# Optimization experiments

Hardware: AMD Instinct MI355X
Metric: run time of the kernel (lower is better)

Reference implementation:

```python
import jax, jax.numpy as jnp
import numpy as np

INPUT_SIZE = 768
HIDDEN = 384


def _gru_dir(x, W_ih, W_hh, b_ih, b_hh, reverse):
    """Single-direction GRU, torch gate order (r, z, n).
    x: [B, S, D] -> outputs [B, S, H]."""
    B = x.shape[0]
    H = W_hh.shape[1]
    # Precompute input projections for all timesteps: [B, S, 3H] -> [S, B, 3H]
    xw = jnp.swapaxes(x @ W_ih.T + b_ih, 0, 1)

    def step(h, xw_t):
        gh = h @ W_hh.T + b_hh
        xr, xz, xn = jnp.split(xw_t, 3, axis=-1)
        hr, hz, hn = jnp.split(gh, 3, axis=-1)
        r = jax.nn.sigmoid(xr + hr)
        z = jax.nn.sigmoid(xz + hz)
        n = jnp.tanh(xn + r * hn)
        h_new = (1.0 - z) * n + z * h
        return h_new, h_new

    h0 = jnp.zeros((B, H), dtype=x.dtype)
    _, hs = jax.lax.scan(step, h0, xw, reverse=reverse)  # [S, B, H]
    return jnp.swapaxes(hs, 0, 1)


def setup_inputs() -> dict:
    key = jax.random.key(0)
    ks = jax.random.split(key, 12)
    B, S, D, H = 32, 512, INPUT_SIZE, HIDDEN
    s_ih = 1.0 / np.sqrt(H)
    u = lambda k, shape: jax.random.uniform(k, shape, jnp.float32, -s_ih, s_ih)
    inp = {
        "ip": jax.random.normal(ks[0], (B, S, D), jnp.float32),
        # forward-direction GRU params
        "W_ih_f": u(ks[1], (3 * H, D)),
        "W_hh_f": u(ks[2], (3 * H, H)),
        "b_ih_f": u(ks[3], (3 * H,)),
        "b_hh_f": u(ks[4], (3 * H,)),
        # backward-direction GRU params
        "W_ih_b": u(ks[5], (3 * H, D)),
        "W_hh_b": u(ks[6], (3 * H, H)),
        "b_ih_b": u(ks[7], (3 * H,)),
        "b_hh_b": u(ks[8], (3 * H,)),
        # sentence attention params (input_dim = 2H)
        "W_attn": u(ks[9], (2 * H, 2 * H)),
        "b_attn": u(ks[10], (2 * H,)),
        "context": jax.random.normal(ks[11], (2 * H,), jnp.float32) * 0.05,
    }
    return inp


def reference(ip, W_ih_f, W_hh_f, b_ih_f, b_hh_f,
              W_ih_b, W_hh_b, b_ih_b, b_hh_b,
              W_attn, b_attn, context):
    # BiGRU encode: concat forward & backward hidden states -> [B, S, 2H]
    h_f = _gru_dir(ip, W_ih_f, W_hh_f, b_ih_f, b_hh_f, reverse=False)
    h_b = _gru_dir(ip, W_ih_b, W_hh_b, b_ih_b, b_hh_b, reverse=True)
    out = jnp.concatenate([h_f, h_b], axis=-1)
    # Additive attention pooling over sentences
    scores = jnp.tanh(out @ W_attn.T + b_attn) @ context  # [B, S]
    attn = jax.nn.softmax(scores, axis=1)
    doc_embeds = jnp.einsum("bs,bsd->bd", attn, out)  # [B, 2H]
    return doc_embeds
```

## Files before the change

kernel.cpp:

```cpp
#include <hip/hip_runtime.h>
#include <hip/hip_fp16.h>

typedef _Float16 half2_t __attribute__((ext_vector_type(2)));
typedef _Float16 half4_t __attribute__((ext_vector_type(4)));
typedef _Float16 half8_t __attribute__((ext_vector_type(8)));
typedef float floatx4 __attribute__((ext_vector_type(4)));

#define B_   32
#define S_   512
#define D_   768
#define H_   384
#define H3_  1152
#define M_   (B_*S_)
#define N2_  (2*H3_)
#define TWOH_ 768
#define NWG_DIR 6
#define JSPAN 64

__device__ __forceinline__ int4 load16_cc(const void* p) {
  int4 r;
  unsigned long long a = (unsigned long long)p;
  asm volatile("global_load_dwordx4 %0, %1, off sc0 sc1\n\t"
               "s_waitcnt vmcnt(0)"
               : "=v"(r) : "v"(a) : "memory");
  return r;
}
__device__ __forceinline__ void load16_cc3(const void* p0, const void* p1, const void* p2,
                                           int4& v0, int4& v1, int4& v2) {
  unsigned long long a0 = (unsigned long long)p0;
  unsigned long long a1 = (unsigned long long)p1;
  unsigned long long a2 = (unsigned long long)p2;
  asm volatile("global_load_dwordx4 %0, %3, off sc0 sc1\n\t"
               "global_load_dwordx4 %1, %4, off sc0 sc1\n\t"
               "global_load_dwordx4 %2, %5, off sc0 sc1\n\t"
               "s_waitcnt vmcnt(0)"
               : "=&v"(v0), "=&v"(v1), "=&v"(v2)
               : "v"(a0), "v"(a1), "v"(a2) : "memory");
}
__device__ __forceinline__ void store8_cc(void* p, int2 v) {
  unsigned long long a = (unsigned long long)p;
  asm volatile("global_store_dwordx2 %0, %1, off sc0 sc1"
               :: "v"(a), "v"(v) : "memory");
}
__device__ __forceinline__ void wait_vm0() {
  asm volatile("s_waitcnt vmcnt(0)" ::: "memory");
}

__global__ void cvt_f32_f16_kernel(const float* __restrict__ src,
                                   _Float16* __restrict__ dst, int n4) {
  int i = blockIdx.x * blockDim.x + threadIdx.x;
  if (i >= n4) return;
  float4 v = ((const float4*)src)[i];
  half4_t h = {(_Float16)v.x, (_Float16)v.y, (_Float16)v.z, (_Float16)v.w};
  ((half4_t*)dst)[i] = h;
}

__global__ __launch_bounds__(256) void gemm_xw_kernel(
    const _Float16* __restrict__ A, const _Float16* __restrict__ Bm,
    const float* __restrict__ bias_f, const float* __restrict__ bias_b,
    _Float16* __restrict__ xw) {
  __shared__ _Float16 As[64][40];
  __shared__ _Float16 Bs[64][40];
  const int m0 = blockIdx.x * 64, n0 = blockIdx.y * 64;
  const int tid = threadIdx.x, lane = tid & 63, w = tid >> 6;
  const int wm = w >> 1, wn = w & 1;
  const int q = lane >> 4, c = lane & 15;
  floatx4 acc[2][2] = {};

  const int t = tid & 127;
  const int srow = t >> 1, skh = (t & 1) * 16;
  const _Float16* gsrc =
      (tid < 128 ? A + (size_t)(m0 + srow) * D_ : Bm + (size_t)(n0 + srow) * D_) + skh;
  _Float16* ldst = (tid < 128) ? &As[srow][skh] : &Bs[srow][skh];

  for (int k0 = 0; k0 < D_; k0 += 32) {
    half8_t v0 = *(const half8_t*)(gsrc + k0);
    half8_t v1 = *(const half8_t*)(gsrc + k0 + 8);
    __syncthreads();
    *(half8_t*)ldst = v0;
    *(half8_t*)(ldst + 8) = v1;
    __syncthreads();
    half8_t a0 = *(const half8_t*)&As[wm * 32 + c][q * 8];
    half8_t a1 = *(const half8_t*)&As[wm * 32 + 16 + c][q * 8];
    half8_t b0 = *(const half8_t*)&Bs[wn * 32 + c][q * 8];
    half8_t b1 = *(const half8_t*)&Bs[wn * 32 + 16 + c][q * 8];
    acc[0][0] = __builtin_amdgcn_mfma_f32_16x16x32_f16(a0, b0, acc[0][0], 0, 0, 0);
    acc[0][1] = __builtin_amdgcn_mfma_f32_16x16x32_f16(a0, b1, acc[0][1], 0, 0, 0);
    acc[1][0] = __builtin_amdgcn_mfma_f32_16x16x32_f16(a1, b0, acc[1][0], 0, 0, 0);
    acc[1][1] = __builtin_amdgcn_mfma_f32_16x16x32_f16(a1, b1, acc[1][1], 0, 0, 0);
  }
  for (int mi = 0; mi < 2; ++mi)
    for (int ni = 0; ni < 2; ++ni)
      for (int r = 0; r < 4; ++r) {
        int m = m0 + wm * 32 + mi * 16 + q * 4 + r;
        int n = n0 + wn * 32 + ni * 16 + c;
        int dir = n >= H3_;
        int nn = n - dir * H3_;
        float bv = dir ? bias_b[nn] : bias_f[nn];
        float vv = acc[mi][ni][r] + bv;
        int s = m & (S_ - 1), bb = m >> 9;
        xw[(((size_t)dir * S_ + s) * B_ + bb) * H3_ + nn] = (_Float16)vv;
      }
}

__global__ __launch_bounds__(512, 2) void gru_mfma_kernel(
    const _Float16* __restrict__ xw,
    const _Float16* __restrict__ Whh,
    const float* __restrict__ bhh_f, const float* __restrict__ bhh_b,
    _Float16* __restrict__ hglob,
    _Float16* __restrict__ out16,
    int* __restrict__ bar) {
  const int wg = blockIdx.x;
  const int dir = wg / NWG_DIR;
  const int wgj = wg % NWG_DIR;
  const int j0w = wgj * JSPAN;
  const int tid = threadIdx.x, lane = tid & 63, w = tid >> 6;
  const int bt = w & 1, jt = w >> 1;
  const int c = lane & 15, q = lane >> 4;

  __shared__ __align__(16) _Float16 hS[32 * 392];
  __shared__ __align__(16) float ghS[3 * 32 * 68];

  half8_t bfr[3][12];
  {
    const int jglob = j0w + jt * 16 + c;
#pragma unroll
    for (int g = 0; g < 3; ++g) {
      const _Float16* wp = Whh + ((size_t)dir * H3_ + g * H_ + jglob) * H_ + q * 8;
#pragma unroll
      for (int kt = 0; kt < 12; ++kt) bfr[g][kt] = *(const half8_t*)(wp + kt * 32);
    }
  }
  const float* bhh = dir ? bhh_b : bhh_f;
  const int gb = tid >> 4, jq = tid & 15;
  const int jg4 = j0w + jq * 4;
  float br[4], bz[4], bn[4], hc[4];
#pragma unroll
  for (int i = 0; i < 4; ++i) {
    br[i] = bhh[jg4 + i];
    bz[i] = bhh[H_ + jg4 + i];
    bn[i] = bhh[2 * H_ + jg4 + i];
    hc[i] = 0.f;
  }
  int* flg = bar + dir * 256;

  for (int step = 0; step < S_; ++step) {
    const int t = dir ? (S_ - 1 - step) : step;
    const int par = step & 1;

    const _Float16* xp = xw + (((size_t)dir * S_ + t) * B_ + gb) * H3_ + jg4;
    half4_t xr4 = *(const half4_t*)(xp);
    half4_t xz4 = *(const half4_t*)(xp + H_);
    half4_t xn4 = *(const half4_t*)(xp + 2 * H_);

    if (step > 0 && w == 0) {
      int v;
      do {
        v = (lane < NWG_DIR)
                ? __hip_atomic_load(&flg[lane * 16], __ATOMIC_RELAXED,
                                    __HIP_MEMORY_SCOPE_AGENT)
                : 0x7fffffff;
      } while (!__all(v >= step));
    }
    __syncthreads();

    {
      const _Float16* hb = hglob + ((size_t)dir * 2 + par) * B_ * H_;
      int g0 = tid, g1 = tid + 512, g2 = tid + 1024;
      int4 v0, v1, v2;
      load16_cc3(hb + (g0 / 48) * H_ + (g0 % 48) * 8,
                 hb + (g1 / 48) * H_ + (g1 % 48) * 8,
                 hb + (g2 / 48) * H_ + (g2 % 48) * 8, v0, v1, v2);
      *(int4*)&hS[(g0 / 48) * 392 + (g0 % 48) * 8] = v0;
      *(int4*)&hS[(g1 / 48) * 392 + (g1 % 48) * 8] = v1;
      *(int4*)&hS[(g2 / 48) * 392 + (g2 % 48) * 8] = v2;
    }
    __syncthreads();

    floatx4 a0 = {}, a1 = {}, a2 = {};
    {
      const _Float16* hrow = &hS[(bt * 16 + c) * 392 + q * 8];
#pragma unroll
      for (int kt = 0; kt < 12; ++kt) {
        half8_t af = *(const half8_t*)(hrow + kt * 32);
        a0 = __builtin_amdgcn_mfma_f32_16x16x32_f16(af, bfr[0][kt], a0, 0, 0, 0);
        a1 = __builtin_amdgcn_mfma_f32_16x16x32_f16(af, bfr[1][kt], a1, 0, 0, 0);
        a2 = __builtin_amdgcn_mfma_f32_16x16x32_f16(af, bfr[2][kt], a2, 0, 0, 0);
      }
    }
#pragma unroll
    for (int r = 0; r < 4; ++r) {
      int brow = bt * 16 + q * 4 + r;
      ghS[(0 * 32 + brow) * 68 + jt * 16 + c] = a0[r];
      ghS[(1 * 32 + brow) * 68 + jt * 16 + c] = a1[r];
      ghS[(2 * 32 + brow) * 68 + jt * 16 + c] = a2[r];
    }
    __syncthreads();

    floatx4 arv = *(floatx4*)&ghS[(0 * 32 + gb) * 68 + jq * 4];
    floatx4 azv = *(floatx4*)&ghS[(1 * 32 + gb) * 68 + jq * 4];
    floatx4 anv = *(floatx4*)&ghS[(2 * 32 + gb) * 68 + jq * 4];
    half4_t hh;
#pragma unroll
    for (int i = 0; i < 4; ++i) {
      float rr = 1.f / (1.f + __expf(-((float)xr4[i] + arv[i] + br[i])));
      float zz = 1.f / (1.f + __expf(-((float)xz4[i] + azv[i] + bz[i])));
      float u = (float)xn4[i] + rr * (anv[i] + bn[i]);
      float e = __expf(-2.f * u);
      float nv = (1.f - e) / (1.f + e);
      hc[i] = (1.f - zz) * nv + zz * hc[i];
      hh[i] = (_Float16)hc[i];
    }
    store8_cc(hglob + (((size_t)dir * 2 + (par ^ 1)) * B_ + gb) * H_ + jg4,
              __builtin_bit_cast(int2, hh));
    wait_vm0();
    __syncthreads();
    if (tid == 0)
      __hip_atomic_store(&flg[wgj * 16], step + 1, __ATOMIC_RELAXED,
                         __HIP_MEMORY_SCOPE_AGENT);
    *(half4_t*)&out16[((size_t)gb * S_ + t) * TWOH_ + dir * H_ + jg4] = hh;
  }
}

__global__ __launch_bounds__(256) void attn_score_kernel(
    const _Float16* __restrict__ A ,
    const _Float16* __restrict__ Bm ,
    const float* __restrict__ b_attn, const float* __restrict__ ctx,
    float* __restrict__ scores) {
  __shared__ _Float16 As[64][40];
  __shared__ _Float16 Bs[64][40];
  const int m0 = blockIdx.x * 64, n0 = blockIdx.y * 64;
  const int tid = threadIdx.x, lane = tid & 63, w = tid >> 6;
  const int wm = w >> 1, wn = w & 1;
  const int q = lane >> 4, c = lane & 15;
  floatx4 acc[2][2] = {};

  const int t = tid & 127;
  const int srow = t >> 1, skh = (t & 1) * 16;
  const _Float16* gsrc =
      (tid < 128 ? A + (size_t)(m0 + srow) * D_ : Bm + (size_t)(n0 + srow) * D_) + skh;
  _Float16* ldst = (tid < 128) ? &As[srow][skh] : &Bs[srow][skh];

  for (int k0 = 0; k0 < D_; k0 += 32) {
    half8_t v0 = *(const half8_t*)(gsrc + k0);
    half8_t v1 = *(const half8_t*)(gsrc + k0 + 8);
    __syncthreads();
    *(half8_t*)ldst = v0;
    *(half8_t*)(ldst + 8) = v1;
    __syncthreads();
    half8_t a0 = *(const half8_t*)&As[wm * 32 + c][q * 8];
    half8_t a1 = *(const half8_t*)&As[wm * 32 + 16 + c][q * 8];
    half8_t b0 = *(const half8_t*)&Bs[wn * 32 + c][q * 8];
    half8_t b1 = *(const half8_t*)&Bs[wn * 32 + 16 + c][q * 8];
    acc[0][0] = __builtin_amdgcn_mfma_f32_16x16x32_f16(a0, b0, acc[0][0], 0, 0, 0);
    acc[0][1] = __builtin_amdgcn_mfma_f32_16x16x32_f16(a0, b1, acc[0][1], 0, 0, 0);
    acc[1][0] = __builtin_amdgcn_mfma_f32_16x16x32_f16(a1, b0, acc[1][0], 0, 0, 0);
    acc[1][1] = __builtin_amdgcn_mfma_f32_16x16x32_f16(a1, b1, acc[1][1], 0, 0, 0);
  }
  for (int mi = 0; mi < 2; ++mi)
    for (int ni = 0; ni < 2; ++ni)
      for (int r = 0; r < 4; ++r) {
        int n = n0 + wn * 32 + ni * 16 + c;
        float vv = tanhf(acc[mi][ni][r] + b_attn[n]) * ctx[n];
        vv += __shfl_xor(vv, 1);
        vv += __shfl_xor(vv, 2);
        vv += __shfl_xor(vv, 4);
        vv += __shfl_xor(vv, 8);
        if (c == 0) {
          int m = m0 + wm * 32 + mi * 16 + q * 4 + r;
          atomicAdd(&scores[m], vv);
        }
      }
}

__global__ __launch_bounds__(256) void softmax_kernel(const float* __restrict__ scores,
                                                      float* __restrict__ attn) {
  const int b = blockIdx.x, tid = threadIdx.x;
  __shared__ float red[8];
  float s0 = scores[b * S_ + tid], s1 = scores[b * S_ + 256 + tid];
  float m = fmaxf(s0, s1);
  for (int off = 1; off < 64; off <<= 1) m = fmaxf(m, __shfl_xor(m, off));
  int wv = tid >> 6;
  if ((tid & 63) == 0) red[wv] = m;
  __syncthreads();
  m = fmaxf(fmaxf(red[0], red[1]), fmaxf(red[2], red[3]));
  float e0 = expf(s0 - m), e1 = expf(s1 - m);
  float sum = e0 + e1;
  for (int off = 1; off < 64; off <<= 1) sum += __shfl_xor(sum, off);
  if ((tid & 63) == 0) red[4 + wv] = sum;
  __syncthreads();
  sum = red[4] + red[5] + red[6] + red[7];
  float inv = 1.0f / sum;
  attn[b * S_ + tid] = e0 * inv;
  attn[b * S_ + 256 + tid] = e1 * inv;
}

__global__ __launch_bounds__(384) void doc_kernel(const float* __restrict__ attn,
                                                  const _Float16* __restrict__ out16,
                                                  float* __restrict__ dout) {
  const int b = blockIdx.x, tid = threadIdx.x;
  __shared__ float at[S_];
  for (int i = tid; i < S_; i += 384) at[i] = attn[b * S_ + i];
  __syncthreads();
  const half2_t* p = (const half2_t*)(out16 + (size_t)b * S_ * TWOH_) + tid;
  float acc0 = 0.f, acc1 = 0.f;
  for (int s = 0; s < S_; ++s) {
    half2_t h = p[(size_t)s * (TWOH_ / 2)];
    float wgt = at[s];
    acc0 += wgt * (float)h.x;
    acc1 += wgt * (float)h.y;
  }
  dout[b * TWOH_ + tid * 2] = acc0;
  dout[b * TWOH_ + tid * 2 + 1] = acc1;
}

extern "C" void kernel_launch(void* const* d_in, const int* in_sizes, int n_in,
                              void* d_out, int out_size, void* d_ws, size_t ws_size,
                              hipStream_t stream) {
  const float* ip     = (const float*)d_in[0];
  const float* W_ih_f = (const float*)d_in[1];
  const float* W_hh_f = (const float*)d_in[2];
  const float* b_ih_f = (const float*)d_in[3];
  const float* b_hh_f_p = (const float*)d_in[4];
  const float* W_ih_b = (const float*)d_in[5];
  const float* W_hh_b = (const float*)d_in[6];
  const float* b_ih_b = (const float*)d_in[7];
  const float* b_hh_b_p = (const float*)d_in[8];
  const float* W_attn = (const float*)d_in[9];
  const float* b_attn = (const float*)d_in[10];
  const float* context = (const float*)d_in[11];
  float* doc = (float*)d_out;

  char* ws = (char*)d_ws;
  size_t off = 0;
  auto alloc = [&](size_t bytes) {
    char* p = ws + off;
    off += (bytes + 255) & ~(size_t)255;
    return p;
  };
  _Float16* ip16    = (_Float16*)alloc((size_t)M_ * D_ * 2);
  _Float16* Wih16   = (_Float16*)alloc((size_t)N2_ * D_ * 2);
  _Float16* Whh16   = (_Float16*)alloc((size_t)2 * H3_ * H_ * 2);
  _Float16* Wattn16 = (_Float16*)alloc((size_t)TWOH_ * TWOH_ * 2);
  _Float16* xw      = (_Float16*)alloc((size_t)2 * S_ * B_ * H3_ * 2);
  _Float16* out16   = (_Float16*)alloc((size_t)B_ * S_ * TWOH_ * 2);
  _Float16* hglob   = (_Float16*)alloc((size_t)2 * 2 * B_ * H_ * 2);
  int*      bar     = (int*)alloc(4096);
  float* scores     = (float*)alloc((size_t)M_ * 4);
  float* attn       = (float*)alloc((size_t)M_ * 4);

  cvt_f32_f16_kernel<<<(M_ * D_ / 4 + 255) / 256, 256, 0, stream>>>(ip, ip16, M_ * D_ / 4);
  cvt_f32_f16_kernel<<<(H3_ * D_ / 4 + 255) / 256, 256, 0, stream>>>(W_ih_f, Wih16, H3_ * D_ / 4);
  cvt_f32_f16_kernel<<<(H3_ * D_ / 4 + 255) / 256, 256, 0, stream>>>(W_ih_b, Wih16 + (size_t)H3_ * D_, H3_ * D_ / 4);
  cvt_f32_f16_kernel<<<(H3_ * H_ / 4 + 255) / 256, 256, 0, stream>>>(W_hh_f, Whh16, H3_ * H_ / 4);
  cvt_f32_f16_kernel<<<(H3_ * H_ / 4 + 255) / 256, 256, 0, stream>>>(W_hh_b, Whh16 + (size_t)H3_ * H_, H3_ * H_ / 4);
  cvt_f32_f16_kernel<<<(TWOH_ * TWOH_ / 4 + 255) / 256, 256, 0, stream>>>(W_attn, Wattn16, TWOH_ * TWOH_ / 4);

  gemm_xw_kernel<<<dim3(M_ / 64, N2_ / 64), 256, 0, stream>>>(ip16, Wih16, b_ih_f, b_ih_b, xw);

  hipMemsetAsync(hglob, 0, (size_t)2 * 2 * B_ * H_ * 2, stream);
  hipMemsetAsync(bar, 0, 4096, stream);
  {
    const _Float16* xw_a = xw;
    const _Float16* whh_a = Whh16;
    const float* bf_a = b_hh_f_p;
    const float* bb_a = b_hh_b_p;
    _Float16* hg_a = hglob;
    _Float16* o16_a = out16;
    int* bar_a = bar;
    void* args[] = {(void*)&xw_a, (void*)&whh_a, (void*)&bf_a, (void*)&bb_a,
                    (void*)&hg_a, (void*)&o16_a, (void*)&bar_a};
    hipLaunchCooperativeKernel((const void*)gru_mfma_kernel, dim3(2 * NWG_DIR),
                               dim3(512), args, 0, stream);
  }

  hipMemsetAsync(scores, 0, (size_t)M_ * 4, stream);
  attn_score_kernel<<<dim3(M_ / 64, TWOH_ / 64), 256, 0, stream>>>(out16, Wattn16, b_attn, context, scores);

  softmax_kernel<<<B_, 256, 0, stream>>>(scores, attn);
  doc_kernel<<<B_, 384, 0, stream>>>(attn, out16, doc);
}
```

Before: 2.216 ms.

## Embed step tags in hidden-state words to replace flag barrier in GRU

The GRU recurrence now stores each pair of fp16 hidden values together with a step counter in one 64-bit word. Readers poll these words directly, so the separate per-workgroup flag array, the wait after the store, the extra block sync and the atomic flag store all go away. This is meant to cut the per-step inter-workgroup synchronisation latency. In addition, the K dimension of the hidden-state matmul is split across wave pairs, which halves the weight registers per thread and adds a two-way shared-memory reduction. The trade-offs are twice the bytes per hidden-state exchange and no zeroing of the exchange buffer, so correctness relies on stale tags never matching.

```diff
diff --git a/kernel.cpp b/kernel.cpp
--- a/kernel.cpp
+++ b/kernel.cpp
@@ -5,6 +5,7 @@
 typedef _Float16 half4_t __attribute__((ext_vector_type(4)));
 typedef _Float16 half8_t __attribute__((ext_vector_type(8)));
 typedef float floatx4 __attribute__((ext_vector_type(4)));
+typedef unsigned long long u64;
 
 #define B_   32
 #define S_   512
@@ -16,34 +17,38 @@
 #define TWOH_ 768
 #define NWG_DIR 6
 #define JSPAN 64
-
-__device__ __forceinline__ int4 load16_cc(const void* p) {
-  int4 r;
-  unsigned long long a = (unsigned long long)p;
-  asm volatile("global_load_dwordx4 %0, %1, off sc0 sc1\n\t"
-               "s_waitcnt vmcnt(0)"
-               : "=v"(r) : "v"(a) : "memory");
-  return r;
-}
-__device__ __forceinline__ void load16_cc3(const void* p0, const void* p1, const void* p2,
-                                           int4& v0, int4& v1, int4& v2) {
-  unsigned long long a0 = (unsigned long long)p0;
-  unsigned long long a1 = (unsigned long long)p1;
-  unsigned long long a2 = (unsigned long long)p2;
-  asm volatile("global_load_dwordx4 %0, %3, off sc0 sc1\n\t"
-               "global_load_dwordx4 %1, %4, off sc0 sc1\n\t"
-               "global_load_dwordx4 %2, %5, off sc0 sc1\n\t"
-               "s_waitcnt vmcnt(0)"
-               : "=&v"(v0), "=&v"(v1), "=&v"(v2)
-               : "v"(a0), "v"(a1), "v"(a2) : "memory");
-}
-__device__ __forceinline__ void store8_cc(void* p, int2 v) {
-  unsigned long long a = (unsigned long long)p;
+#define NCHUNK 6144
+
+__device__ __forceinline__ void store8_cc(void* p, u64 v) {
   asm volatile("global_store_dwordx2 %0, %1, off sc0 sc1"
-               :: "v"(a), "v"(v) : "memory");
-}
-__device__ __forceinline__ void wait_vm0() {
-  asm volatile("s_waitcnt vmcnt(0)" ::: "memory");
+               :: "v"((u64)p), "v"(v) : "memory");
+}
+__device__ __forceinline__ void load12_cc(const u64* base, int tid, u64 v[12]) {
+  u64 a0 = (u64)(base + tid);
+  u64 a1 = a0 + 1 * 4096, a2 = a0 + 2 * 4096, a3 = a0 + 3 * 4096;
+  u64 a4 = a0 + 4 * 4096, a5 = a0 + 5 * 4096, a6 = a0 + 6 * 4096;
+  u64 a7 = a0 + 7 * 4096, a8 = a0 + 8 * 4096, a9 = a0 + 9 * 4096;
+  u64 a10 = a0 + 10 * 4096, a11 = a0 + 11 * 4096;
+  asm volatile(
+      "global_load_dwordx2 %0, %12, off sc0 sc1\n\t"
+      "global_load_dwordx2 %1, %13, off sc0 sc1\n\t"
+      "global_load_dwordx2 %2, %14, off sc0 sc1\n\t"
+      "global_load_dwordx2 %3, %15, off sc0 sc1\n\t"
+      "global_load_dwordx2 %4, %16, off sc0 sc1\n\t"
+      "global_load_dwordx2 %5, %17, off sc0 sc1\n\t"
+      "global_load_dwordx2 %6, %18, off sc0 sc1\n\t"
+      "global_load_dwordx2 %7, %19, off sc0 sc1\n\t"
+      "global_load_dwordx2 %8, %20, off sc0 sc1\n\t"
+      "global_load_dwordx2 %9, %21, off sc0 sc1\n\t"
+      "global_load_dwordx2 %10, %22, off sc0 sc1\n\t"
+      "global_load_dwordx2 %11, %23, off sc0 sc1\n\t"
+      "s_waitcnt vmcnt(0)"
+      : "=&v"(v[0]), "=&v"(v[1]), "=&v"(v[2]), "=&v"(v[3]),
+        "=&v"(v[4]), "=&v"(v[5]), "=&v"(v[6]), "=&v"(v[7]),
+        "=&v"(v[8]), "=&v"(v[9]), "=&v"(v[10]), "=&v"(v[11])
+      : "v"(a0), "v"(a1), "v"(a2), "v"(a3), "v"(a4), "v"(a5),
+        "v"(a6), "v"(a7), "v"(a8), "v"(a9), "v"(a10), "v"(a11)
+      : "memory");
 }
 
 __global__ void cvt_f32_f16_kernel(const float* __restrict__ src,
@@ -107,28 +112,29 @@
     const _Float16* __restrict__ xw,
     const _Float16* __restrict__ Whh,
     const float* __restrict__ bhh_f, const float* __restrict__ bhh_b,
-    _Float16* __restrict__ hglob,
-    _Float16* __restrict__ out16,
-    int* __restrict__ bar) {
+    u64* __restrict__ hglob,
+    _Float16* __restrict__ out16) {
   const int wg = blockIdx.x;
-  const int dir = wg / NWG_DIR;
-  const int wgj = wg % NWG_DIR;
+  const int dir = wg / NWG_DIR, wgj = wg % NWG_DIR;
   const int j0w = wgj * JSPAN;
   const int tid = threadIdx.x, lane = tid & 63, w = tid >> 6;
-  const int bt = w & 1, jt = w >> 1;
+  const int kh = w & 1, jt = w >> 1;
   const int c = lane & 15, q = lane >> 4;
 
-  __shared__ __align__(16) _Float16 hS[32 * 392];
-  __shared__ __align__(16) float ghS[3 * 32 * 68];
-
-  half8_t bfr[3][12];
+  __shared__ __align__(16) char smemS[2 * 3 * 32 * 68 * 4];
+  _Float16* hS = (_Float16*)smemS;
+  typedef float ghArr[3][32][68];
+  ghArr* ghS = (ghArr*)smemS;
+
+  half8_t bfr[3][6];
   {
     const int jglob = j0w + jt * 16 + c;
 #pragma unroll
     for (int g = 0; g < 3; ++g) {
-      const _Float16* wp = Whh + ((size_t)dir * H3_ + g * H_ + jglob) * H_ + q * 8;
-#pragma unroll
-      for (int kt = 0; kt < 12; ++kt) bfr[g][kt] = *(const half8_t*)(wp + kt * 32);
+      const _Float16* wp =
+          Whh + ((size_t)dir * H3_ + g * H_ + jglob) * H_ + kh * 192 + q * 8;
+#pragma unroll
+      for (int kt2 = 0; kt2 < 6; ++kt2) bfr[g][kt2] = *(const half8_t*)(wp + kt2 * 32);
     }
   }
   const float* bhh = dir ? bhh_b : bhh_f;
@@ -142,64 +148,76 @@
     bn[i] = bhh[2 * H_ + jg4 + i];
     hc[i] = 0.f;
   }
-  int* flg = bar + dir * 256;
+  int gbch[12], gjp[12];
+#pragma unroll
+  for (int k = 0; k < 12; ++k) {
+    int id = tid + k * 512;
+    gbch[k] = id / 192;
+    gjp[k] = id % 192;
+  }
+
+  for (int i = tid; i < 1568; i += 512) ((int4*)smemS)[i] = (int4){0, 0, 0, 0};
 
   for (int step = 0; step < S_; ++step) {
     const int t = dir ? (S_ - 1 - step) : step;
-    const int par = step & 1;
 
     const _Float16* xp = xw + (((size_t)dir * S_ + t) * B_ + gb) * H3_ + jg4;
-    half4_t xr4 = *(const half4_t*)(xp);
+    half4_t xr4 = *(const half4_t*)xp;
     half4_t xz4 = *(const half4_t*)(xp + H_);
     half4_t xn4 = *(const half4_t*)(xp + 2 * H_);
 
-    if (step > 0 && w == 0) {
-      int v;
-      do {
-        v = (lane < NWG_DIR)
-                ? __hip_atomic_load(&flg[lane * 16], __ATOMIC_RELAXED,
-                                    __HIP_MEMORY_SCOPE_AGENT)
-                : 0x7fffffff;
-      } while (!__all(v >= step));
-    }
-    __syncthreads();
-
+    u64 v[12];
+    if (step > 0) {
+      const u64* slotp = hglob + ((size_t)dir * 2 + (step & 1)) * NCHUNK;
+      for (;;) {
+        load12_cc(slotp, tid, v);
+        bool ok = true;
+#pragma unroll
+        for (int k = 0; k < 12; ++k) ok &= ((unsigned)v[k] == (unsigned)step);
+        if (ok) break;
+      }
+    }
+    __syncthreads();
+    if (step > 0) {
+#pragma unroll
+      for (int k = 0; k < 12; ++k)
+        *(int*)&hS[gbch[k] * 392 + gjp[k] * 2] = (int)(v[k] >> 32);
+    }
+    __syncthreads();
+
+    floatx4 acc[3][2] = {};
     {
-      const _Float16* hb = hglob + ((size_t)dir * 2 + par) * B_ * H_;
-      int g0 = tid, g1 = tid + 512, g2 = tid + 1024;
-      int4 v0, v1, v2;
-      load16_cc3(hb + (g0 / 48) * H_ + (g0 % 48) * 8,
-                 hb + (g1 / 48) * H_ + (g1 % 48) * 8,
-                 hb + (g2 / 48) * H_ + (g2 % 48) * 8, v0, v1, v2);
-      *(int4*)&hS[(g0 / 48) * 392 + (g0 % 48) * 8] = v0;
-      *(int4*)&hS[(g1 / 48) * 392 + (g1 % 48) * 8] = v1;
-      *(int4*)&hS[(g2 / 48) * 392 + (g2 % 48) * 8] = v2;
-    }
-    __syncthreads();
-
-    floatx4 a0 = {}, a1 = {}, a2 = {};
+      const _Float16* hrow = &hS[c * 392 + kh * 192 + q * 8];
+#pragma unroll
+      for (int kt2 = 0; kt2 < 6; ++kt2) {
+        half8_t a0 = *(const half8_t*)(hrow + kt2 * 32);
+        half8_t a1 = *(const half8_t*)(hrow + 16 * 392 + kt2 * 32);
+#pragma unroll
+        for (int g = 0; g < 3; ++g) {
+          acc[g][0] = __builtin_amdgcn_mfma_f32_16x16x32_f16(a0, bfr[g][kt2], acc[g][0], 0, 0, 0);
+          acc[g][1] = __builtin_amdgcn_mfma_f32_16x16x32_f16(a1, bfr[g][kt2], acc[g][1], 0, 0, 0);
+        }
+      }
+    }
+    __syncthreads();
+#pragma unroll
+    for (int g = 0; g < 3; ++g)
+#pragma unroll
+      for (int bt = 0; bt < 2; ++bt)
+#pragma unroll
+        for (int r = 0; r < 4; ++r)
+          ghS[kh][g][bt * 16 + q * 4 + r][jt * 16 + c] = acc[g][bt][r];
+    __syncthreads();
+
+    floatx4 arv = *(floatx4*)&ghS[0][0][gb][jq * 4];
+    floatx4 azv = *(floatx4*)&ghS[0][1][gb][jq * 4];
+    floatx4 anv = *(floatx4*)&ghS[0][2][gb][jq * 4];
     {
-      const _Float16* hrow = &hS[(bt * 16 + c) * 392 + q * 8];
-#pragma unroll
-      for (int kt = 0; kt < 12; ++kt) {
-        half8_t af = *(const half8_t*)(hrow + kt * 32);
-        a0 = __builtin_amdgcn_mfma_f32_16x16x32_f16(af, bfr[0][kt], a0, 0, 0, 0);
-        a1 = __builtin_amdgcn_mfma_f32_16x16x32_f16(af, bfr[1][kt], a1, 0, 0, 0);
-        a2 = __builtin_amdgcn_mfma_f32_16x16x32_f16(af, bfr[2][kt], a2, 0, 0, 0);
-      }
-    }
-#pragma unroll
-    for (int r = 0; r < 4; ++r) {
-      int brow = bt * 16 + q * 4 + r;
-      ghS[(0 * 32 + brow) * 68 + jt * 16 + c] = a0[r];
-      ghS[(1 * 32 + brow) * 68 + jt * 16 + c] = a1[r];
-      ghS[(2 * 32 + brow) * 68 + jt * 16 + c] = a2[r];
-    }
-    __syncthreads();
-
-    floatx4 arv = *(floatx4*)&ghS[(0 * 32 + gb) * 68 + jq * 4];
-    floatx4 azv = *(floatx4*)&ghS[(1 * 32 + gb) * 68 + jq * 4];
-    floatx4 anv = *(floatx4*)&ghS[(2 * 32 + gb) * 68 + jq * 4];
+      floatx4 t0 = *(floatx4*)&ghS[1][0][gb][jq * 4];
+      floatx4 t1 = *(floatx4*)&ghS[1][1][gb][jq * 4];
+      floatx4 t2 = *(floatx4*)&ghS[1][2][gb][jq * 4];
+      arv += t0; azv += t1; anv += t2;
+    }
     half4_t hh;
 #pragma unroll
     for (int i = 0; i < 4; ++i) {
@@ -211,13 +229,16 @@
       hc[i] = (1.f - zz) * nv + zz * hc[i];
       hh[i] = (_Float16)hc[i];
     }
-    store8_cc(hglob + (((size_t)dir * 2 + (par ^ 1)) * B_ + gb) * H_ + jg4,
-              __builtin_bit_cast(int2, hh));
-    wait_vm0();
-    __syncthreads();
-    if (tid == 0)
-      __hip_atomic_store(&flg[wgj * 16], step + 1, __ATOMIC_RELAXED,
-                         __HIP_MEMORY_SCOPE_AGENT);
+    {
+      u64* wslot = hglob + ((size_t)dir * 2 + ((step + 1) & 1)) * NCHUNK;
+      int cb = gb * 192 + (jg4 >> 1);
+      half2_t p0; p0.x = hh[0]; p0.y = hh[1];
+      half2_t p1; p1.x = hh[2]; p1.y = hh[3];
+      u64 c0 = ((u64)__builtin_bit_cast(unsigned, p0) << 32) | (unsigned)(step + 1);
+      u64 c1 = ((u64)__builtin_bit_cast(unsigned, p1) << 32) | (unsigned)(step + 1);
+      store8_cc(wslot + cb, c0);
+      store8_cc(wslot + cb + 1, c1);
+    }
     *(half4_t*)&out16[((size_t)gb * S_ + t) * TWOH_ + dir * H_ + jg4] = hh;
   }
 }
@@ -344,8 +365,7 @@
   _Float16* Wattn16 = (_Float16*)alloc((size_t)TWOH_ * TWOH_ * 2);
   _Float16* xw      = (_Float16*)alloc((size_t)2 * S_ * B_ * H3_ * 2);
   _Float16* out16   = (_Float16*)alloc((size_t)B_ * S_ * TWOH_ * 2);
-  _Float16* hglob   = (_Float16*)alloc((size_t)2 * 2 * B_ * H_ * 2);
-  int*      bar     = (int*)alloc(4096);
+  u64*      hglob   = (u64*)alloc((size_t)2 * 2 * NCHUNK * 8);
   float* scores     = (float*)alloc((size_t)M_ * 4);
   float* attn       = (float*)alloc((size_t)M_ * 4);
 
@@ -358,18 +378,15 @@
 
   gemm_xw_kernel<<<dim3(M_ / 64, N2_ / 64), 256, 0, stream>>>(ip16, Wih16, b_ih_f, b_ih_b, xw);
 
-  hipMemsetAsync(hglob, 0, (size_t)2 * 2 * B_ * H_ * 2, stream);
-  hipMemsetAsync(bar, 0, 4096, stream);
   {
     const _Float16* xw_a = xw;
     const _Float16* whh_a = Whh16;
     const float* bf_a = b_hh_f_p;
     const float* bb_a = b_hh_b_p;
-    _Float16* hg_a = hglob;
+    u64* hg_a = hglob;
     _Float16* o16_a = out16;
-    int* bar_a = bar;
     void* args[] = {(void*)&xw_a, (void*)&whh_a, (void*)&bf_a, (void*)&bb_a,
-                    (void*)&hg_a, (void*)&o16_a, (void*)&bar_a};
+                    (void*)&hg_a, (void*)&o16_a};
     hipLaunchCooperativeKernel((const void*)gru_mfma_kernel, dim3(2 * NWG_DIR),
                                dim3(512), args, 0, stream);
   }
```

Result: slower. 2.406 ms (+8.6%).
